# Kernel tuning notes

Hardware: AMD Instinct MI355X
Metric: run time of the kernel (lower is better)

## Reference

```python
import jax, jax.numpy as jnp
import numpy as np

HEADS = 5 - 1  # 4 attention heads (GPSConv heads=4)


def _bn(x, g, b, eps=1e-5):
    # BatchNorm1d, training-mode math (biased variance), matches torch normalization
    mu = x.mean(0)
    var = x.var(0)
    return g * (x - mu) * jax.lax.rsqrt(var + eps) + b


def _forward(x, t, freqs, t_fc1_W, t_fc1_b, t_fc2_W, t_fc2_b, node_W, node_b,
             tproj_W, tproj_b, tcat_W, tcat_b, pen_g, pen_b, pel_W, pel_b,
             cat_W, cat_b, conv_Wg, gru_Wih, gru_bih, gru_Whh, gru_bhh,
             attn_Wqkv, attn_bqkv, attn_Wo, attn_bo, bn_g, bn_b,
             mlp_W1, mlp_b1, mlp_W2, mlp_b2, out_W, out_b):
    B, C, Hh, Ww = x.shape
    HD = node_W.shape[1]          # hidden_dim = 64
    DH = HD // HEADS              # per-head dim = 16
    WL = pen_g.shape[0]           # walk_length = 20

    xf = x.reshape(B, -1)                              # [B, D]
    h = xf @ node_W + node_b                           # node_proj

    # TimeEmbedding: t @ freqs -> sin/cos -> MLP, then time_proj
    tp = t.reshape(B, 1) * freqs.reshape(1, -1)        # [B, nf]
    two_pi = jnp.asarray(2.0 * np.pi, x.dtype)
    te = jnp.concatenate([jnp.sin(two_pi * tp), jnp.cos(two_pi * tp)], axis=-1)
    te = jax.nn.silu(te @ t_fc1_W + t_fc1_b) @ t_fc2_W + t_fc2_b
    h_time = te @ tproj_W + tproj_b
    h = jnp.concatenate([h, h_time], axis=-1) @ tcat_W + tcat_b  # time_cat_proj

    # Fully-connected graph incl. self-loops: A = 1 everywhere, deg = B.
    # Random-walk PE: P = A/deg has all entries 1/B; P is idempotent (P@P = P),
    # hence diag(P^k) = diag(P) = 1/B for every k in 1..walk_length.
    A = jnp.ones((B, B), x.dtype)
    P = A / A.sum(1, keepdims=True)
    pe = jnp.broadcast_to(jnp.diagonal(P)[:, None], (B, WL))
    pe = _bn(pe, pen_g, pen_b)                         # pe_norm (batch stats)
    h = jnp.concatenate([h, pe @ pel_W + pel_b], axis=-1) @ cat_W + cat_b

    inv_sqrt = jnp.asarray(1.0 / np.sqrt(DH), x.dtype)
    for l in range(conv_Wg.shape[0]):                  # 5 GPSConv layers
        # --- GatedGraphConv (num_layers=1): message, add-aggregate, GRU ---
        m = A @ (h @ conv_Wg[l])                       # sum of messages from all src nodes
        gi = m @ gru_Wih[l] + gru_bih[l]               # [B, 3H]
        gh = h @ gru_Whh[l] + gru_bhh[l]
        ir, iz, inn = jnp.split(gi, 3, axis=-1)
        hr, hz, hn = jnp.split(gh, 3, axis=-1)
        r = jax.nn.sigmoid(ir + hr)
        z = jax.nn.sigmoid(iz + hz)
        n = jnp.tanh(inn + r * hn)
        hc = (1.0 - z) * n + z * h                     # GRUCell output
        h1 = _bn(hc + h, bn_g[l, 0], bn_b[l, 0])       # residual + norm1

        # --- global multihead self-attention over the single dense batch ---
        qkv = h @ attn_Wqkv[l] + attn_bqkv[l]
        q, k, v = jnp.split(qkv, 3, axis=-1)
        q = q.reshape(B, HEADS, DH).transpose(1, 0, 2)  # [h, B, d]
        k = k.reshape(B, HEADS, DH).transpose(1, 0, 2)
        v = v.reshape(B, HEADS, DH).transpose(1, 0, 2)
        att = jax.nn.softmax(jnp.einsum('hqd,hkd->hqk', q, k) * inv_sqrt, axis=-1)
        o = jnp.einsum('hqk,hkd->hqd', att, v).transpose(1, 0, 2).reshape(B, HD)
        o = o @ attn_Wo[l] + attn_bo[l]
        h2 = _bn(o + h, bn_g[l, 1], bn_b[l, 1])        # residual + norm2

        s = h1 + h2
        s = s + (jax.nn.relu(s @ mlp_W1[l] + mlp_b1[l]) @ mlp_W2[l] + mlp_b2[l])
        h = _bn(s, bn_g[l, 2], bn_b[l, 2])             # norm3

    return (h @ out_W + out_b).reshape(B, C, Hh, Ww)


def setup_inputs() -> dict:
    key = jax.random.key(0)
    B, C, H, W = 2048, 4, 32, 32
    D = C * H * W                 # 4096
    HD, PE, WL, L = 64, 16, 20, 5
    NF, TH, TC = 8, 64, 64
    ks = iter(jax.random.split(key, 40))

    def rn(shape, s=0.05):
        return jax.random.normal(next(ks), shape, jnp.float32) * s

    return {
        'x': jax.random.normal(next(ks), (B, C, H, W), jnp.float32),
        't': jax.random.uniform(next(ks), (B,), jnp.float32),
        'freqs': rn((NF,), 1.0),
        't_fc1_W': rn((2 * NF, TH)), 't_fc1_b': rn((TH,)),
        't_fc2_W': rn((TH, TC)), 't_fc2_b': rn((TC,)),
        'node_W': rn((D, HD), 0.02), 'node_b': rn((HD,)),
        'tproj_W': rn((TC, HD)), 'tproj_b': rn((HD,)),
        'tcat_W': rn((2 * HD, HD)), 'tcat_b': rn((HD,)),
        'pen_g': jnp.ones((WL,), jnp.float32), 'pen_b': jnp.zeros((WL,), jnp.float32),
        'pel_W': rn((WL, PE)), 'pel_b': rn((PE,)),
        'cat_W': rn((HD + PE, HD)), 'cat_b': rn((HD,)),
        'conv_Wg': rn((L, HD, HD)),
        'gru_Wih': rn((L, HD, 3 * HD)), 'gru_bih': rn((L, 3 * HD)),
        'gru_Whh': rn((L, HD, 3 * HD)), 'gru_bhh': rn((L, 3 * HD)),
        'attn_Wqkv': rn((L, HD, 3 * HD)), 'attn_bqkv': rn((L, 3 * HD)),
        'attn_Wo': rn((L, HD, HD)), 'attn_bo': rn((L, HD)),
        'bn_g': jnp.ones((L, 3, HD), jnp.float32), 'bn_b': jnp.zeros((L, 3, HD), jnp.float32),
        'mlp_W1': rn((L, HD, 2 * HD)), 'mlp_b1': rn((L, 2 * HD)),
        'mlp_W2': rn((L, 2 * HD, HD)), 'mlp_b2': rn((L, HD)),
        'out_W': rn((HD, D)), 'out_b': rn((D,)),
    }


def reference(x, t, freqs, t_fc1_W, t_fc1_b, t_fc2_W, t_fc2_b, node_W, node_b,
              tproj_W, tproj_b, tcat_W, tcat_b, pen_g, pen_b, pel_W, pel_b,
              cat_W, cat_b, conv_Wg, gru_Wih, gru_bih, gru_Whh, gru_bhh,
              attn_Wqkv, attn_bqkv, attn_Wo, attn_bo, bn_g, bn_b,
              mlp_W1, mlp_b1, mlp_W2, mlp_b2, out_W, out_b):
    return _forward(x, t, freqs, t_fc1_W, t_fc1_b, t_fc2_W, t_fc2_b, node_W, node_b,
                    tproj_W, tproj_b, tcat_W, tcat_b, pen_g, pen_b, pel_W, pel_b,
                    cat_W, cat_b, conv_Wg, gru_Wih, gru_bih, gru_Whh, gru_bhh,
                    attn_Wqkv, attn_bqkv, attn_Wo, attn_bo, bn_g, bn_b,
                    mlp_W1, mlp_b1, mlp_W2, mlp_b2, out_W, out_b)
```

## Files before the change

### kernel.cpp

```cpp
#include <hip/hip_runtime.h>

#define NB 2048
#define HDM 64
#define NLAY 5

typedef __bf16 bf16x8 __attribute__((ext_vector_type(8)));
typedef float v4f __attribute__((ext_vector_type(4)));

__device__ __forceinline__ float sigmoidf_(float x){ return 1.f/(1.f+__expf(-x)); }
__device__ __forceinline__ float tanhfast_(float x){
  x = fminf(fmaxf(x, -15.f), 15.f);
  float e = __expf(2.f*x);
  return (e-1.f)/(e+1.f);
}
__device__ __forceinline__ unsigned short f2b_rne(float f){
  unsigned u = __float_as_uint(f);
  unsigned r = u + 0x7FFFu + ((u>>16)&1u);
  return (unsigned short)(r>>16);
}
__device__ __forceinline__ unsigned pk2(float a, float b){
  unsigned ua = (__float_as_uint(a) + 0x8000u) >> 16;
  unsigned ub = (__float_as_uint(b) + 0x8000u) & 0xFFFF0000u;
  return ua | ub;
}

__global__ __launch_bounds__(256) void k_pre(
    const float* __restrict__ x, const float* __restrict__ tt,
    const float* __restrict__ freqs,
    const float* __restrict__ fc1W, const float* __restrict__ fc1b,
    const float* __restrict__ fc2W, const float* __restrict__ fc2b,
    const float* __restrict__ tprojW, const float* __restrict__ tprojb,
    const float* __restrict__ nodeW,
    float* __restrict__ h0p, float* __restrict__ htime,
    float* __restrict__ zero_region)
{
  __shared__ float xs[16*260];
  __shared__ float tb0[128];
  __shared__ float tb1[128];
  const int t = threadIdx.x, blk = blockIdx.x;
  const int r = t>>6, c = t&63;

  if (blk == 0){
    for (int i = t; i < 320 + 1920; i += 256) zero_region[i] = 0.f;
  }

  {
    const int row = blk*2 + (r&1);
    const float tv = tt[row];
    if (r < 2){
      float te[16];
      #pragma unroll
      for (int j=0;j<8;++j){
        float sv, cv;
        __sincosf(6.28318530717958647692f*tv*freqs[j], &sv, &cv);
        te[j]=sv; te[j+8]=cv;
      }
      float a = fc1b[c];
      #pragma unroll
      for (int j=0;j<16;++j) a += te[j]*fc1W[j*64+c];
      tb0[r*64+c] = a*sigmoidf_(a);
    }
    __syncthreads();
    if (r < 2){
      float b2 = fc2b[c];
      #pragma unroll 8
      for (int k=0;k<64;++k) b2 += tb0[r*64+k]*fc2W[k*64+c];
      tb1[r*64+c] = b2;
    }
    __syncthreads();
    if (r < 2){
      float hti = tprojb[c];
      #pragma unroll 8
      for (int k=0;k<64;++k) hti += tb1[r*64+k]*tprojW[k*64+c];
      htime[row*64+c] = hti;
    }
  }

  const int rg = blk>>3, kq = blk&7;
  const int rows0 = rg*16, k0 = kq*512;
  const int col4 = (t&15)*4;
  const int rq4  = ((t>>4)&3)*4;
  const int ksub = (t>>6)*64;

  float4 a0={0,0,0,0}, a1={0,0,0,0}, a2={0,0,0,0}, a3={0,0,0,0};

  for (int ch=0; ch<2; ++ch){
    __syncthreads();
    #pragma unroll
    for (int i=0;i<4;++i){
      int fi = t + 256*i;
      int xr = fi>>6, kk = (fi&63)<<2;
      *(float4*)&xs[xr*260+kk] = *(const float4*)&x[(size_t)(rows0+xr)*4096 + k0 + ch*256 + kk];
    }
    __syncthreads();
    const float* wp = &nodeW[(size_t)(k0 + ch*256 + ksub)*64 + col4];
    const float* xp = &xs[rq4*260 + ksub];
    #pragma unroll 8
    for (int kk=0; kk<64; ++kk){
      float4 w  = *(const float4*)&wp[kk*64];
      float x0 = xp[kk];
      float x1 = xp[260+kk];
      float x2 = xp[520+kk];
      float x3 = xp[780+kk];
      a0.x += x0*w.x; a0.y += x0*w.y; a0.z += x0*w.z; a0.w += x0*w.w;
      a1.x += x1*w.x; a1.y += x1*w.y; a1.z += x1*w.z; a1.w += x1*w.w;
      a2.x += x2*w.x; a2.y += x2*w.y; a2.z += x2*w.z; a2.w += x2*w.w;
      a3.x += x3*w.x; a3.y += x3*w.y; a3.z += x3*w.z; a3.w += x3*w.w;
    }
  }
  __syncthreads();
  {
    const int kqi = t>>6;
    *(float4*)&xs[(kqi*16 + rq4 + 0)*64 + col4] = a0;
    *(float4*)&xs[(kqi*16 + rq4 + 1)*64 + col4] = a1;
    *(float4*)&xs[(kqi*16 + rq4 + 2)*64 + col4] = a2;
    *(float4*)&xs[(kqi*16 + rq4 + 3)*64 + col4] = a3;
  }
  __syncthreads();
  {
    const int row = t>>4, c4 = (t&15)*4;
    float4 s = {0,0,0,0};
    #pragma unroll
    for (int q=0;q<4;++q){
      float4 v = *(const float4*)&xs[(q*16+row)*64 + c4];
      s.x+=v.x; s.y+=v.y; s.z+=v.z; s.w+=v.w;
    }
    *(float4*)&h0p[(size_t)kq*(NB*HDM) + (rows0+row)*64 + c4] = s;
  }
}

__global__ __launch_bounds__(256) void k_assemble(
    const float* __restrict__ h0p, const float* __restrict__ htime,
    const float* __restrict__ nodeb,
    const float* __restrict__ tcatW, const float* __restrict__ tcatb,
    const float* __restrict__ penb, const float* __restrict__ pelW,
    const float* __restrict__ pelb,
    const float* __restrict__ catW, const float* __restrict__ catb,
    float* __restrict__ hbuf)
{
  __shared__ float sa[256];
  __shared__ float sb[256];
  __shared__ float cvec[64];
  const int t = threadIdx.x, blk = blockIdx.x;
  const int r = t>>6, c = t&63;
  const int row = blk*4 + r;

  if (r==0){
    float pl[16];
    #pragma unroll
    for (int j=0;j<16;++j){
      float a = pelb[j];
      for (int w=0;w<20;++w) a += penb[w]*pelW[w*16+j];
      pl[j]=a;
    }
    float a = catb[c];
    #pragma unroll
    for (int j=0;j<16;++j) a += pl[j]*catW[(64+j)*64+c];
    cvec[c]=a;
  }
  float h0 = nodeb[c];
  #pragma unroll
  for (int q=0;q<8;++q) h0 += h0p[(size_t)q*(NB*HDM) + row*64 + c];
  sa[t] = h0;
  sb[t] = htime[row*64+c];
  __syncthreads();
  float a = tcatb[c];
  #pragma unroll 4
  for (int k=0;k<64;++k){
    a += sa[r*64+k]*tcatW[k*64+c];
    a += sb[r*64+k]*tcatW[(64+k)*64+c];
  }
  __syncthreads();
  sa[t] = a;
  __syncthreads();
  float hv = cvec[c];
  #pragma unroll 8
  for (int k=0;k<64;++k) hv += sa[r*64+k]*catW[k*64+c];
  hbuf[row*64+c] = hv;
}

__global__ __launch_bounds__(256) void k_A(
    const float* __restrict__ smlp,
    const float* __restrict__ bnaccPrev,
    const float* __restrict__ gPrev, const float* __restrict__ bPrev,
    float* __restrict__ hbuf, float* __restrict__ hsumL,
    const float* __restrict__ Whh, const float* __restrict__ bhh,
    const float* __restrict__ Wq,  const float* __restrict__ bq,
    float* __restrict__ gh,
    unsigned short* __restrict__ Qb, unsigned short* __restrict__ Kb,
    unsigned short* __restrict__ Vt, int first)
{
  __shared__ float sa[8*64];
  const int t = threadIdx.x, blk = blockIdx.x;
  const int row0 = blk*8;

  #pragma unroll
  for (int i=0;i<2;++i){
    int idx = t + 256*i;
    int rl = idx>>6, c = idx&63;
    int row = row0 + rl;
    float hv;
    if (first){
      hv = hbuf[row*64+c];
    } else {
      float mu = bnaccPrev[256+c]*(1.f/NB);
      float va = bnaccPrev[320+c]*(1.f/NB) - mu*mu;
      hv = gPrev[c]*(smlp[row*64+c]-mu)*rsqrtf(va+1e-5f)+bPrev[c];
      hbuf[row*64+c] = hv;
    }
    sa[idx] = hv;
  }
  __syncthreads();
  if (t<64){
    float s = 0.f;
    #pragma unroll
    for (int rl=0;rl<8;++rl) s += sa[rl*64+t];
    atomicAdd(&hsumL[t], s);
  }
  if (t < 192){
    const int cc = t;
    float ag[8], aq[8];
    float bh = bhh[cc], bq_ = bq[cc];
    #pragma unroll
    for (int rl=0;rl<8;++rl){ ag[rl]=bh; aq[rl]=bq_; }
    #pragma unroll 4
    for (int k=0;k<64;++k){
      float wh = Whh[k*192+cc];
      float wq = Wq [k*192+cc];
      #pragma unroll
      for (int rl=0;rl<8;++rl){
        float hk = sa[rl*64+k];
        ag[rl] += hk*wh;
        aq[rl] += hk*wq;
      }
    }
    #pragma unroll
    for (int rl=0;rl<8;++rl){
      int rw = row0 + rl;
      gh[(size_t)rw*192+cc] = ag[rl];
      float aqv = aq[rl];
      if (cc < 64){
        int hd = cc>>4, dh = cc&15;
        size_t base = ((size_t)(hd<<11) + rw)*32;
        Qb[base+dh] = f2b_rne(aqv*0.25f);
        Qb[base+16+dh] = 0;
      } else if (cc < 128){
        int c2 = cc-64, hd = c2>>4, dh = c2&15;
        size_t base = ((size_t)(hd<<11) + rw)*32;
        Kb[base+dh] = f2b_rne(aqv);
        Kb[base+16+dh] = 0;
      } else {
        int c2 = cc-128, hd = c2>>4, dh = c2&15;
        Vt[((size_t)(hd*16+dh))*2048 + rw] = f2b_rne(aqv);
      }
    }
  }
}

__global__ __launch_bounds__(256) void k_attn(
    const unsigned short* __restrict__ Qb, const unsigned short* __restrict__ Kb,
    const unsigned short* __restrict__ Vt,
    float* __restrict__ o_out)
{
  __shared__ unsigned short Pl[4*640];
  __shared__ float Os[4*272];
  __shared__ float ms[64], ls[64];
  const int t = threadIdx.x;
  const int w = t>>6, lane = t&63;
  const int q15 = lane & 15, quad = lane >> 4;
  const int b = blockIdx.x;
  const int qt = b & 127, head = b>>7;
  const int qrow = qt*16 + q15;
  const int key00 = w*512;
  unsigned short* Plw = &Pl[w*640];

  const bf16x8 qf = *(const bf16x8*)&Qb[(((size_t)(head<<11))+qrow)*32 + quad*8];
  const unsigned short* Kb_h = Kb + ((size_t)(head<<11))*32;
  const unsigned short* Vrow = Vt + ((size_t)(head*16+q15))*2048;

  v4f O = {0.f,0.f,0.f,0.f};
  float m = -1e30f, lsum = 0.f;

  bf16x8 kf0 = *(const bf16x8*)&Kb_h[(size_t)(key00 + q15)*32 + quad*8];
  bf16x8 kf1 = *(const bf16x8*)&Kb_h[(size_t)(key00 + 16 + q15)*32 + quad*8];
  bf16x8 vf  = *(const bf16x8*)&Vrow[key00 + quad*8];

  for (int c=0; c<16; ++c){
    bf16x8 nk0, nk1, nv;
    if (c < 15){
      int nk = key00 + (c+1)*32;
      nk0 = *(const bf16x8*)&Kb_h[(size_t)(nk + q15)*32 + quad*8];
      nk1 = *(const bf16x8*)&Kb_h[(size_t)(nk + 16 + q15)*32 + quad*8];
      nv  = *(const bf16x8*)&Vrow[nk + quad*8];
    }
    v4f z = {0.f,0.f,0.f,0.f};
    v4f s0 = __builtin_amdgcn_mfma_f32_16x16x32_bf16(kf0, qf, z, 0,0,0);
    v4f s1 = __builtin_amdgcn_mfma_f32_16x16x32_bf16(kf1, qf, z, 0,0,0);
    float cmax = fmaxf(fmaxf(fmaxf(s0[0],s0[1]),fmaxf(s0[2],s0[3])),
                       fmaxf(fmaxf(s1[0],s1[1]),fmaxf(s1[2],s1[3])));
    cmax = fmaxf(cmax, __shfl_xor(cmax,16,64));
    cmax = fmaxf(cmax, __shfl_xor(cmax,32,64));
    float mnew = fmaxf(m, cmax);
    float alpha = __expf(m - mnew);
    float p0=__expf(s0[0]-mnew), p1=__expf(s0[1]-mnew), p2=__expf(s0[2]-mnew), p3=__expf(s0[3]-mnew);
    float p4=__expf(s1[0]-mnew), p5=__expf(s1[1]-mnew), p6=__expf(s1[2]-mnew), p7=__expf(s1[3]-mnew);
    lsum = alpha*lsum + ((p0+p1)+(p2+p3)+((p4+p5)+(p6+p7)));
    m = mnew;
    O[0]*=alpha; O[1]*=alpha; O[2]*=alpha; O[3]*=alpha;
    *(uint2*)&Plw[q15*40 + quad*4]      = make_uint2(pk2(p0,p1), pk2(p2,p3));
    *(uint2*)&Plw[q15*40 + 16 + quad*4] = make_uint2(pk2(p4,p5), pk2(p6,p7));
    asm volatile("s_waitcnt lgkmcnt(0)" ::: "memory");
    bf16x8 pf = *(const bf16x8*)&Plw[q15*40 + quad*8];
    O = __builtin_amdgcn_mfma_f32_16x16x32_bf16(vf, pf, O, 0,0,0);
    kf0 = nk0; kf1 = nk1; vf = nv;
  }
  lsum += __shfl_xor(lsum,16,64);
  lsum += __shfl_xor(lsum,32,64);
  #pragma unroll
  for (int j=0;j<4;++j) Os[w*272 + q15*17 + quad*4 + j] = O[j];
  if (quad==0){ ms[w*16+q15]=m; ls[w*16+q15]=lsum; }
  __syncthreads();
  {
    const int dh = t&15, q = t>>4;
    float m0=ms[q], m1=ms[16+q], m2=ms[32+q], m3=ms[48+q];
    float mm = fmaxf(fmaxf(m0,m1),fmaxf(m2,m3));
    float a0=__expf(m0-mm), a1=__expf(m1-mm), a2=__expf(m2-mm), a3=__expf(m3-mm);
    float ll = a0*ls[q]+a1*ls[16+q]+a2*ls[32+q]+a3*ls[48+q];
    float oo = a0*Os[q*17+dh] + a1*Os[272+q*17+dh] + a2*Os[544+q*17+dh] + a3*Os[816+q*17+dh];
    o_out[(size_t)(qt*16+q)*64 + head*16 + dh] = oo / ll;
  }
}

__global__ __launch_bounds__(256) void k_B2(
    const float* __restrict__ hbuf, const float* __restrict__ gh,
    const float* __restrict__ hsumL, const float* __restrict__ o_out,
    const float* __restrict__ Wg,   const float* __restrict__ Wih,
    const float* __restrict__ bih,  const float* __restrict__ Wo,
    const float* __restrict__ bo,
    float* __restrict__ s1, float* __restrict__ s2, float* __restrict__ bnaccL)
{
  __shared__ float sa[8*64];
  __shared__ float os[8*64];
  __shared__ float smv_[64];
  __shared__ float sgi[192];
  __shared__ float Sb1[8*64];
  __shared__ float Sb2[8*64];
  const int t = threadIdx.x, blk = blockIdx.x;
  const int row0 = blk*8;

  if (t<64){
    float a=0.f;
    #pragma unroll 8
    for (int k=0;k<64;++k) a += hsumL[k]*Wg[k*64+t];
    smv_[t]=a;
  }
  #pragma unroll
  for (int i=0;i<2;++i){
    int idx = t + 256*i;
    int rl = idx>>6, c = idx&63;
    sa[idx] = hbuf[(size_t)(row0+rl)*64+c];
    os[idx] = o_out[(size_t)(row0+rl)*64+c];
  }
  __syncthreads();
  if (t<192){
    float a = bih[t];
    #pragma unroll 8
    for (int k=0;k<64;++k) a += smv_[k]*Wih[k*192+t];
    sgi[t]=a;
  }
  __syncthreads();

  const int c = t&63, rg = t>>6;
  float o2a = bo[c], o2b = bo[c];
  #pragma unroll 4
  for (int k=0;k<64;++k){
    float w = Wo[k*64+c];
    o2a += os[(rg*2  )*64+k]*w;
    o2b += os[(rg*2+1)*64+k]*w;
  }
  #pragma unroll
  for (int i=0;i<2;++i){
    int rl = rg*2 + i;
    int row = row0 + rl;
    float o2 = i ? o2b : o2a;
    float hv = sa[rl*64+c];
    float s2v = o2 + hv;
    float ir = sgi[c]      + gh[(size_t)row*192+c];
    float iz = sgi[64+c]   + gh[(size_t)row*192+64+c];
    float inn = sgi[128+c];
    float hn  = gh[(size_t)row*192+128+c];
    float rr_ = sigmoidf_(ir);
    float zz  = sigmoidf_(iz);
    float nn  = tanhfast_(inn + rr_*hn);
    float s1v = (1.f-zz)*nn + zz*hv + hv;
    s1[(size_t)row*64+c] = s1v;
    s2[(size_t)row*64+c] = s2v;
    Sb1[rl*64+c] = s1v;
    Sb2[rl*64+c] = s2v;
  }
  __syncthreads();
  if (t<64){
    float a=0.f,aq=0.f,b=0.f,bq2=0.f;
    #pragma unroll
    for (int rl=0;rl<8;++rl){
      float v1 = Sb1[rl*64+t], v2 = Sb2[rl*64+t];
      a+=v1; aq+=v1*v1; b+=v2; bq2+=v2*v2;
    }
    atomicAdd(&bnaccL[t],a);     atomicAdd(&bnaccL[64+t],aq);
    atomicAdd(&bnaccL[128+t],b); atomicAdd(&bnaccL[192+t],bq2);
  }
}

__global__ __launch_bounds__(256) void k_C(
    const float* __restrict__ s1, const float* __restrict__ s2,
    const float* __restrict__ bngL, const float* __restrict__ bnbL,
    const float* __restrict__ W1, const float* __restrict__ b1,
    const float* __restrict__ W2, const float* __restrict__ b2,
    float* __restrict__ smlp, float* __restrict__ bnaccL)
{
  __shared__ float sa[8*64];
  __shared__ float sh[8*128];
  __shared__ float S2[8*64];
  const int t = threadIdx.x, blk = blockIdx.x;
  const int row0 = blk*8;

  #pragma unroll
  for (int i=0;i<2;++i){
    int idx = t + 256*i;
    int rl = idx>>6, c = idx&63;
    int row = row0 + rl;
    float mu1 = bnaccL[c]*(1.f/NB);
    float va1 = bnaccL[64+c]*(1.f/NB) - mu1*mu1;
    float mu2 = bnaccL[128+c]*(1.f/NB);
    float va2 = bnaccL[192+c]*(1.f/NB) - mu2*mu2;
    float h1 = bngL[c]*(s1[(size_t)row*64+c]-mu1)*rsqrtf(va1+1e-5f)+bnbL[c];
    float h2 = bngL[64+c]*(s2[(size_t)row*64+c]-mu2)*rsqrtf(va2+1e-5f)+bnbL[64+c];
    sa[idx] = h1+h2;
  }
  __syncthreads();
  {
    const int hj = t&127, rgq = t>>7;
    float a0v=b1[hj], a1v=b1[hj], a2v=b1[hj], a3v=b1[hj];
    #pragma unroll 4
    for (int k=0;k<64;++k){
      float w = W1[k*128+hj];
      a0v += sa[(rgq*4  )*64+k]*w;
      a1v += sa[(rgq*4+1)*64+k]*w;
      a2v += sa[(rgq*4+2)*64+k]*w;
      a3v += sa[(rgq*4+3)*64+k]*w;
    }
    sh[(rgq*4  )*128+hj] = fmaxf(a0v,0.f);
    sh[(rgq*4+1)*128+hj] = fmaxf(a1v,0.f);
    sh[(rgq*4+2)*128+hj] = fmaxf(a2v,0.f);
    sh[(rgq*4+3)*128+hj] = fmaxf(a3v,0.f);
  }
  __syncthreads();
  {
    const int c = t&63, rg = t>>6;
    float moa = b2[c], mob = b2[c];
    #pragma unroll 4
    for (int k=0;k<128;++k){
      float w = W2[k*64+c];
      moa += sh[(rg*2  )*128+k]*w;
      mob += sh[(rg*2+1)*128+k]*w;
    }
    #pragma unroll
    for (int i=0;i<2;++i){
      int rl = rg*2+i;
      float smv2 = sa[rl*64+c] + (i ? mob : moa);
      smlp[(size_t)(row0+rl)*64+c] = smv2;
      S2[rl*64+c] = smv2;
    }
  }
  __syncthreads();
  if (t<64){
    float a=0.f,aq=0.f;
    #pragma unroll
    for (int rl=0;rl<8;++rl){ float v=S2[rl*64+t]; a+=v; aq+=v*v; }
    atomicAdd(&bnaccL[256+t],a); atomicAdd(&bnaccL[320+t],aq);
  }
}

__global__ __launch_bounds__(256) void k_out(
  const float* __restrict__ smlp, const float* __restrict__ bnacc4,
  const float* __restrict__ g4, const float* __restrict__ b4,
  const float* __restrict__ outW, const float* __restrict__ outb,
  float* __restrict__ out)
{
  __shared__ float hsT[64*20];
  const int t = threadIdx.x, blk = blockIdx.x;
  const int rg = blk>>2, cg = blk&3;
  const int rows0 = rg*16;
  #pragma unroll
  for (int i=0;i<4;++i){
    int idx = t + 256*i;
    int k = idx&63, rr = idx>>6;
    float mu = bnacc4[256+k]*(1.f/NB);
    float va = bnacc4[320+k]*(1.f/NB)-mu*mu;
    hsT[k*20+rr] = g4[k]*(smlp[(size_t)(rows0+rr)*64+k]-mu)*rsqrtf(va+1e-5f)+b4[k];
  }
  __syncthreads();
  const int cc = cg*1024 + t*4;
  float4 acc[16];
  {
    float4 bv = *(const float4*)&outb[cc];
    #pragma unroll
    for (int rr=0;rr<16;++rr) acc[rr]=bv;
  }
  #pragma unroll 4
  for (int k=0;k<64;++k){
    float4 w = *(const float4*)&outW[(size_t)k*4096+cc];
    const float4* hp = (const float4*)&hsT[k*20];
    float4 h0=hp[0], h1=hp[1], h2=hp[2], h3=hp[3];
    acc[0].x+=h0.x*w.x;  acc[0].y+=h0.x*w.y;  acc[0].z+=h0.x*w.z;  acc[0].w+=h0.x*w.w;
    acc[1].x+=h0.y*w.x;  acc[1].y+=h0.y*w.y;  acc[1].z+=h0.y*w.z;  acc[1].w+=h0.y*w.w;
    acc[2].x+=h0.z*w.x;  acc[2].y+=h0.z*w.y;  acc[2].z+=h0.z*w.z;  acc[2].w+=h0.z*w.w;
    acc[3].x+=h0.w*w.x;  acc[3].y+=h0.w*w.y;  acc[3].z+=h0.w*w.z;  acc[3].w+=h0.w*w.w;
    acc[4].x+=h1.x*w.x;  acc[4].y+=h1.x*w.y;  acc[4].z+=h1.x*w.z;  acc[4].w+=h1.x*w.w;
    acc[5].x+=h1.y*w.x;  acc[5].y+=h1.y*w.y;  acc[5].z+=h1.y*w.z;  acc[5].w+=h1.y*w.w;
    acc[6].x+=h1.z*w.x;  acc[6].y+=h1.z*w.y;  acc[6].z+=h1.z*w.z;  acc[6].w+=h1.z*w.w;
    acc[7].x+=h1.w*w.x;  acc[7].y+=h1.w*w.y;  acc[7].z+=h1.w*w.z;  acc[7].w+=h1.w*w.w;
    acc[8].x+=h2.x*w.x;  acc[8].y+=h2.x*w.y;  acc[8].z+=h2.x*w.z;  acc[8].w+=h2.x*w.w;
    acc[9].x+=h2.y*w.x;  acc[9].y+=h2.y*w.y;  acc[9].z+=h2.y*w.z;  acc[9].w+=h2.y*w.w;
    acc[10].x+=h2.z*w.x; acc[10].y+=h2.z*w.y; acc[10].z+=h2.z*w.z; acc[10].w+=h2.z*w.w;
    acc[11].x+=h2.w*w.x; acc[11].y+=h2.w*w.y; acc[11].z+=h2.w*w.z; acc[11].w+=h2.w*w.w;
    acc[12].x+=h3.x*w.x; acc[12].y+=h3.x*w.y; acc[12].z+=h3.x*w.z; acc[12].w+=h3.x*w.w;
    acc[13].x+=h3.y*w.x; acc[13].y+=h3.y*w.y; acc[13].z+=h3.y*w.z; acc[13].w+=h3.y*w.w;
    acc[14].x+=h3.z*w.x; acc[14].y+=h3.z*w.y; acc[14].z+=h3.z*w.z; acc[14].w+=h3.z*w.w;
    acc[15].x+=h3.w*w.x; acc[15].y+=h3.w*w.y; acc[15].z+=h3.w*w.z; acc[15].w+=h3.w*w.w;
  }
  #pragma unroll
  for (int rr=0;rr<16;++rr)
    *(float4*)&out[(size_t)(rows0+rr)*4096+cc] = acc[rr];
}

extern "C" void kernel_launch(void* const* d_in, const int* in_sizes, int n_in,
                              void* d_out, int out_size, void* d_ws, size_t ws_size,
                              hipStream_t stream)
{
  (void)in_sizes; (void)n_in; (void)out_size; (void)ws_size;
  const float* x      = (const float*)d_in[0];
  const float* tt     = (const float*)d_in[1];
  const float* freqs  = (const float*)d_in[2];
  const float* fc1W   = (const float*)d_in[3];
  const float* fc1b   = (const float*)d_in[4];
  const float* fc2W   = (const float*)d_in[5];
  const float* fc2b   = (const float*)d_in[6];
  const float* nodeW  = (const float*)d_in[7];
  const float* nodeb  = (const float*)d_in[8];
  const float* tprojW = (const float*)d_in[9];
  const float* tprojb = (const float*)d_in[10];
  const float* tcatW  = (const float*)d_in[11];
  const float* tcatb  = (const float*)d_in[12];
  const float* penb   = (const float*)d_in[14];
  const float* pelW   = (const float*)d_in[15];
  const float* pelb   = (const float*)d_in[16];
  const float* catW   = (const float*)d_in[17];
  const float* catb   = (const float*)d_in[18];
  const float* convWg = (const float*)d_in[19];
  const float* gruWih = (const float*)d_in[20];
  const float* grubih = (const float*)d_in[21];
  const float* gruWhh = (const float*)d_in[22];
  const float* grubhh = (const float*)d_in[23];
  const float* Wqkv   = (const float*)d_in[24];
  const float* bqkv   = (const float*)d_in[25];
  const float* Wo     = (const float*)d_in[26];
  const float* bo     = (const float*)d_in[27];
  const float* bng    = (const float*)d_in[28];
  const float* bnb    = (const float*)d_in[29];
  const float* W1     = (const float*)d_in[30];
  const float* b1     = (const float*)d_in[31];
  const float* W2     = (const float*)d_in[32];
  const float* b2     = (const float*)d_in[33];
  const float* outW   = (const float*)d_in[34];
  const float* outb   = (const float*)d_in[35];

  float* ws = (float*)d_ws;
  float* htime = ws;
  float* hbuf  = htime + 131072;
  float* gh    = hbuf + 131072;
  float* s1    = gh + 393216;
  float* s2    = s1 + 131072;
  float* smlp  = s2 + 131072;
  float* o_out = smlp + 131072;
  float* hsum  = o_out + 131072;
  float* bnacc = hsum + 320;
  unsigned short* Qb = (unsigned short*)(bnacc + 1920);
  unsigned short* Kb = Qb + 262144;
  unsigned short* Vt = Kb + 262144;
  float* h0p  = (float*)(Vt + 65536);

  dim3 Blk(256);

  k_pre<<<dim3(1024), Blk, 0, stream>>>(x, tt, freqs, fc1W, fc1b, fc2W, fc2b,
                                        tprojW, tprojb, nodeW, h0p, htime, hsum);

  k_assemble<<<dim3(512), Blk, 0, stream>>>(h0p, htime, nodeb, tcatW, tcatb,
                                            penb, pelW, pelb, catW, catb, hbuf);

  for (int l=0; l<NLAY; ++l){
    const float* bnaccPrev = (l==0) ? bnacc : bnacc + (l-1)*384;
    const float* gPrev = (l==0) ? bng : bng + (l-1)*192 + 128;
    const float* bPrev = (l==0) ? bnb : bnb + (l-1)*192 + 128;
    k_A<<<dim3(256), Blk, 0, stream>>>(smlp, bnaccPrev, gPrev, bPrev,
                                       hbuf, hsum + l*64,
                                       gruWhh + l*12288, grubhh + l*192,
                                       Wqkv + l*12288, bqkv + l*192,
                                       gh, Qb, Kb, Vt, (l==0) ? 1 : 0);
    k_attn<<<dim3(512), Blk, 0, stream>>>(Qb, Kb, Vt, o_out);
    k_B2<<<dim3(256), Blk, 0, stream>>>(hbuf, gh, hsum + l*64, o_out,
                                        convWg + l*4096, gruWih + l*12288, grubih + l*192,
                                        Wo + l*4096, bo + l*64,
                                        s1, s2, bnacc + l*384);
    k_C<<<dim3(256), Blk, 0, stream>>>(s1, s2, bng + l*192, bnb + l*192,
                                       W1 + l*8192, b1 + l*128, W2 + l*8192, b2 + l*64,
                                       smlp, bnacc + l*384);
  }

  k_out<<<dim3(512), Blk, 0, stream>>>(smlp, bnacc + 4*384, bng + 896, bnb + 896,
                                       outW, outb, (float*)d_out);
}
```

Measured before the change: 523.5 us.

## Fuse all stages into one persistent megakernel with grid-wide barriers

```diff
diff --git a/kernel.cpp b/kernel.cpp
--- a/kernel.cpp
+++ b/kernel.cpp
@@ -24,514 +24,438 @@
   return ua | ub;
 }
 
-__global__ __launch_bounds__(256) void k_pre(
-    const float* __restrict__ x, const float* __restrict__ tt,
-    const float* __restrict__ freqs,
-    const float* __restrict__ fc1W, const float* __restrict__ fc1b,
-    const float* __restrict__ fc2W, const float* __restrict__ fc2b,
-    const float* __restrict__ tprojW, const float* __restrict__ tprojb,
-    const float* __restrict__ nodeW,
-    float* __restrict__ h0p, float* __restrict__ htime,
-    float* __restrict__ zero_region)
+struct MP {
+  const float *x, *tt, *freqs, *fc1W, *fc1b, *fc2W, *fc2b, *tprojW, *tprojb;
+  const float *nodeW, *nodeb, *tcatW, *tcatb, *penb, *pelW, *pelb, *catW, *catb;
+  const float *convWg, *gruWih, *grubih, *gruWhh, *grubhh;
+  const float *Wqkv, *bqkv, *Wo, *bo, *bng, *bnb, *W1, *b1, *W2, *b2, *outW, *outb;
+  float *out;
+  unsigned *cnt;
+  float *hsum;
+  float *bnacc;
+  unsigned short *Kb, *Vt;
+  float *h0p;
+  float *smlpG;
+};
+
+__device__ __forceinline__ void gbar(unsigned* cnt, unsigned& ph){
+  __syncthreads();
+  if (threadIdx.x == 0){
+    ph += 1;
+    unsigned tgt = ph * 256u;
+    __hip_atomic_fetch_add(cnt, 1u, __ATOMIC_ACQ_REL, __HIP_MEMORY_SCOPE_AGENT);
+    while (__hip_atomic_load(cnt, __ATOMIC_ACQUIRE, __HIP_MEMORY_SCOPE_AGENT) < tgt)
+      __builtin_amdgcn_s_sleep(2);
+  }
+  __syncthreads();
+}
+
+__global__ __launch_bounds__(512) void k_mega(MP p)
 {
-  __shared__ float xs[16*260];
-  __shared__ float tb0[128];
-  __shared__ float tb1[128];
+  __shared__ float LDSf[11264];
+  float* hL    = LDSf;
+  float* ghL   = LDSf + 512;
+  float* qL    = LDSf + 2048;
+  float* smlpL = LDSf + 2560;
+  float* TR    = LDSf + 3072;
+
   const int t = threadIdx.x, blk = blockIdx.x;
-  const int r = t>>6, c = t&63;
-
-  if (blk == 0){
-    for (int i = t; i < 320 + 1920; i += 256) zero_region[i] = 0.f;
+  const int row0 = blk*8;
+  unsigned bph = 0;
+
+  {
+    const int rt = blk>>1, kq = blk&1;
+    const int rows0 = rt*16, k0 = kq*2048;
+    const int col4 = (t&15)*4, rq4 = ((t>>4)&3)*4, ks = t>>6;
+    float4 a0={0,0,0,0}, a1={0,0,0,0}, a2={0,0,0,0}, a3={0,0,0,0};
+    for (int ch=0; ch<8; ++ch){
+      __syncthreads();
+      #pragma unroll
+      for (int i=0;i<2;++i){
+        int fi = t + 512*i;
+        int xr = fi>>6, kk = (fi&63)<<2;
+        *(float4*)&TR[xr*260+kk] = *(const float4*)&p.x[(size_t)(rows0+xr)*4096 + k0 + ch*256 + kk];
+      }
+      __syncthreads();
+      const float* wp = &p.nodeW[(size_t)(k0 + ch*256 + ks*32)*64 + col4];
+      const float* xp = &TR[rq4*260 + ks*32];
+      #pragma unroll 8
+      for (int kk=0; kk<32; ++kk){
+        float4 w = *(const float4*)&wp[kk*64];
+        float x0 = xp[kk], x1 = xp[260+kk], x2 = xp[520+kk], x3 = xp[780+kk];
+        a0.x += x0*w.x; a0.y += x0*w.y; a0.z += x0*w.z; a0.w += x0*w.w;
+        a1.x += x1*w.x; a1.y += x1*w.y; a1.z += x1*w.z; a1.w += x1*w.w;
+        a2.x += x2*w.x; a2.y += x2*w.y; a2.z += x2*w.z; a2.w += x2*w.w;
+        a3.x += x3*w.x; a3.y += x3*w.y; a3.z += x3*w.z; a3.w += x3*w.w;
+      }
+    }
+    __syncthreads();
+    *(float4*)&TR[ks*1024 + (rq4+0)*64 + col4] = a0;
+    *(float4*)&TR[ks*1024 + (rq4+1)*64 + col4] = a1;
+    *(float4*)&TR[ks*1024 + (rq4+2)*64 + col4] = a2;
+    *(float4*)&TR[ks*1024 + (rq4+3)*64 + col4] = a3;
+    __syncthreads();
+    if (t < 256){
+      int row = t>>4, c4 = (t&15)*4;
+      float4 s = {0,0,0,0};
+      #pragma unroll
+      for (int q=0;q<8;++q){
+        float4 v = *(const float4*)&TR[q*1024 + row*64 + c4];
+        s.x+=v.x; s.y+=v.y; s.z+=v.z; s.w+=v.w;
+      }
+      *(float4*)&p.h0p[(size_t)kq*(NB*64) + (size_t)(rows0+row)*64 + c4] = s;
+    }
   }
-
-  {
-    const int row = blk*2 + (r&1);
-    const float tv = tt[row];
-    if (r < 2){
+  gbar(p.cnt, bph);
+
+  for (int l=0; l<NLAY; ++l){
+    if (l == 0){
+      float* tb0 = TR;        float* tb1 = TR+512;
+      float* htL = TR+1024;   float* h0L = TR+1536;
+      float* hcat= TR+2048;   float* cvec= TR+2560;
+      const int r = t>>6, c = t&63;
+      const int row = row0 + r;
+      float tv = p.tt[row];
       float te[16];
       #pragma unroll
       for (int j=0;j<8;++j){
         float sv, cv;
-        __sincosf(6.28318530717958647692f*tv*freqs[j], &sv, &cv);
+        __sincosf(6.28318530717958647692f*tv*p.freqs[j], &sv, &cv);
         te[j]=sv; te[j+8]=cv;
       }
-      float a = fc1b[c];
+      float a = p.fc1b[c];
       #pragma unroll
-      for (int j=0;j<16;++j) a += te[j]*fc1W[j*64+c];
+      for (int j=0;j<16;++j) a += te[j]*p.fc1W[j*64+c];
       tb0[r*64+c] = a*sigmoidf_(a);
+      h0L[r*64+c] = p.nodeb[c] + p.h0p[(size_t)row*64+c] + p.h0p[(size_t)NB*64 + (size_t)row*64+c];
+      if (t < 64){
+        float pl[16];
+        #pragma unroll
+        for (int j=0;j<16;++j){
+          float pa = p.pelb[j];
+          for (int wv=0;wv<20;++wv) pa += p.penb[wv]*p.pelW[wv*16+j];
+          pl[j]=pa;
+        }
+        float cv = p.catb[t];
+        #pragma unroll
+        for (int j=0;j<16;++j) cv += pl[j]*p.catW[(64+j)*64+t];
+        cvec[t]=cv;
+      }
+      __syncthreads();
+      float b2v = p.fc2b[c];
+      #pragma unroll 8
+      for (int k=0;k<64;++k) b2v += tb0[r*64+k]*p.fc2W[k*64+c];
+      tb1[r*64+c] = b2v;
+      __syncthreads();
+      float ht = p.tprojb[c];
+      #pragma unroll 8
+      for (int k=0;k<64;++k) ht += tb1[r*64+k]*p.tprojW[k*64+c];
+      htL[r*64+c] = ht;
+      __syncthreads();
+      float ac = p.tcatb[c];
+      #pragma unroll 4
+      for (int k=0;k<64;++k){
+        ac += h0L[r*64+k]*p.tcatW[k*64+c];
+        ac += htL[r*64+k]*p.tcatW[(64+k)*64+c];
+      }
+      hcat[r*64+c] = ac;
+      __syncthreads();
+      float hv = cvec[c];
+      #pragma unroll 8
+      for (int k=0;k<64;++k) hv += hcat[r*64+k]*p.catW[k*64+c];
+      hL[r*64+c] = hv;
+      __syncthreads();
+      if (t < 64){
+        float s = 0.f;
+        #pragma unroll
+        for (int rl=0;rl<8;++rl) s += hL[rl*64+t];
+        atomicAdd(&p.hsum[t], s);
+      }
+    } else {
+      const float* stp = p.bnacc + (l-1)*384;
+      const float* gP = p.bng + (l-1)*192 + 128;
+      const float* bP = p.bnb + (l-1)*192 + 128;
+      const int c = t&63, rg = t>>6;
+      float mu = stp[256+c]*(1.f/NB);
+      float va = stp[320+c]*(1.f/NB) - mu*mu;
+      hL[rg*64+c] = gP[c]*(smlpL[rg*64+c]-mu)*rsqrtf(va+1e-5f)+bP[c];
+      __syncthreads();
+    }
+    {
+      int grp = -1, cc = 0;
+      if (t < 192){ grp = 0; cc = t; }
+      else if (t >= 256 && t < 448){ grp = 1; cc = t-256; }
+      if (grp >= 0){
+        const float* Whh = p.gruWhh + l*12288;
+        const float* Wq  = p.Wqkv  + l*12288;
+        float ag[4], aq[4];
+        float bh = p.grubhh[l*192+cc], bqv = p.bqkv[l*192+cc];
+        #pragma unroll
+        for (int rl=0;rl<4;++rl){ ag[rl]=bh; aq[rl]=bqv; }
+        const int rb = grp*4;
+        #pragma unroll 4
+        for (int k=0;k<64;++k){
+          float wh = Whh[k*192+cc];
+          float wq = Wq [k*192+cc];
+          #pragma unroll
+          for (int rl=0;rl<4;++rl){
+            float hk = hL[(rb+rl)*64+k];
+            ag[rl] += hk*wh;
+            aq[rl] += hk*wq;
+          }
+        }
+        #pragma unroll
+        for (int rl=0;rl<4;++rl){
+          int r4 = rb+rl, rw = row0 + r4;
+          ghL[r4*192+cc] = ag[rl];
+          float av = aq[rl];
+          if (cc < 64){
+            qL[r4*64+cc] = av;
+          } else if (cc < 128){
+            int c2 = cc-64, hd = c2>>4, dh = c2&15;
+            size_t base = ((size_t)(hd<<11) + rw)*32;
+            p.Kb[base+dh] = f2b_rne(av);
+            p.Kb[base+16+dh] = 0;
+          } else {
+            int c2 = cc-128, hd = c2>>4, dh = c2&15;
+            p.Vt[((size_t)(hd*16+dh))*2048 + rw] = f2b_rne(av);
+          }
+        }
+      }
+    }
+    gbar(p.cnt, bph);
+
+    {
+      float* smv = TR;     float* gi = TR+64;
+      if (t < 64){
+        const float* Wg = p.convWg + l*4096;
+        float a = 0.f;
+        if (l == 0){
+          #pragma unroll 8
+          for (int k=0;k<64;++k) a += p.hsum[k]*Wg[k*64+t];
+        } else {
+          const float* bP = p.bnb + (l-1)*192 + 128;
+          #pragma unroll 8
+          for (int k=0;k<64;++k) a += (2048.f*bP[k])*Wg[k*64+t];
+        }
+        smv[t]=a;
+      }
+      __syncthreads();
+      if (t < 192){
+        const float* Wih = p.gruWih + l*12288;
+        float a = p.grubih[l*192+t];
+        #pragma unroll 8
+        for (int k=0;k<64;++k) a += smv[k]*Wih[k*192+t];
+        gi[t]=a;
+      }
+      {
+        const int w = t>>6, lane = t&63;
+        const int q15 = lane&15, quad = lane>>4;
+        const int head = w>>1, e = w&1;
+        const int key00 = e*1024;
+        unsigned short* Plw = (unsigned short*)(TR+256) + w*640;
+        bf16x8 qf;
+        {
+          unsigned short* qp = (unsigned short*)&qf;
+          #pragma unroll
+          for (int j=0;j<8;++j){
+            int dh = quad*8+j;
+            float v = (q15 < 8 && dh < 16) ? qL[q15*64 + head*16 + dh]*0.25f : 0.f;
+            qp[j] = f2b_rne(v);
+          }
+        }
+        const unsigned short* Kb_h = p.Kb + ((size_t)(head<<11))*32;
+        const unsigned short* Vrow = p.Vt + ((size_t)(head*16+q15))*2048;
+        v4f O = {0.f,0.f,0.f,0.f};
+        float m = -1e30f, lsum = 0.f;
+        bf16x8 kf0 = *(const bf16x8*)&Kb_h[(size_t)(key00 + q15)*32 + quad*8];
+        bf16x8 kf1 = *(const bf16x8*)&Kb_h[(size_t)(key00 + 16 + q15)*32 + quad*8];
+        bf16x8 vf  = *(const bf16x8*)&Vrow[key00 + quad*8];
+        for (int c=0; c<32; ++c){
+          bf16x8 nk0, nk1, nv;
+          if (c < 31){
+            int nk = key00 + (c+1)*32;
+            nk0 = *(const bf16x8*)&Kb_h[(size_t)(nk + q15)*32 + quad*8];
+            nk1 = *(const bf16x8*)&Kb_h[(size_t)(nk + 16 + q15)*32 + quad*8];
+            nv  = *(const bf16x8*)&Vrow[nk + quad*8];
+          }
+          v4f z = {0.f,0.f,0.f,0.f};
+          v4f s0 = __builtin_amdgcn_mfma_f32_16x16x32_bf16(kf0, qf, z, 0,0,0);
+          v4f s1 = __builtin_amdgcn_mfma_f32_16x16x32_bf16(kf1, qf, z, 0,0,0);
+          float cmax = fmaxf(fmaxf(fmaxf(s0[0],s0[1]),fmaxf(s0[2],s0[3])),
+                             fmaxf(fmaxf(s1[0],s1[1]),fmaxf(s1[2],s1[3])));
+          cmax = fmaxf(cmax, __shfl_xor(cmax,16,64));
+          cmax = fmaxf(cmax, __shfl_xor(cmax,32,64));
+          float mnew = fmaxf(m, cmax);
+          float alpha = __expf(m - mnew);
+          float p0=__expf(s0[0]-mnew), p1=__expf(s0[1]-mnew), p2=__expf(s0[2]-mnew), p3=__expf(s0[3]-mnew);
+          float p4=__expf(s1[0]-mnew), p5=__expf(s1[1]-mnew), p6=__expf(s1[2]-mnew), p7=__expf(s1[3]-mnew);
+          lsum = alpha*lsum + ((p0+p1)+(p2+p3)+((p4+p5)+(p6+p7)));
+          m = mnew;
+          O[0]*=alpha; O[1]*=alpha; O[2]*=alpha; O[3]*=alpha;
+          *(uint2*)&Plw[q15*40 + quad*4]      = make_uint2(pk2(p0,p1), pk2(p2,p3));
+          *(uint2*)&Plw[q15*40 + 16 + quad*4] = make_uint2(pk2(p4,p5), pk2(p6,p7));
+          asm volatile("s_waitcnt lgkmcnt(0)" ::: "memory");
+          bf16x8 pf = *(const bf16x8*)&Plw[q15*40 + quad*8];
+          O = __builtin_amdgcn_mfma_f32_16x16x32_bf16(vf, pf, O, 0,0,0);
+          kf0 = nk0; kf1 = nk1; vf = nv;
+        }
+        lsum += __shfl_xor(lsum,16,64);
+        lsum += __shfl_xor(lsum,32,64);
+        float* Os = TR+2816; float* ms = TR+4992; float* ls = TR+5120;
+        #pragma unroll
+        for (int j=0;j<4;++j) Os[w*272 + q15*17 + quad*4 + j] = O[j];
+        if (quad==0){ ms[w*16+q15]=m; ls[w*16+q15]=lsum; }
+      }
+      __syncthreads();
+      {
+        float* Os = TR+2816; float* ms = TR+4992; float* ls = TR+5120; float* oL = TR+5248;
+        const int q = t>>6, c = t&63;
+        const int head = c>>4, dh = c&15;
+        const int w0 = head*2, w1 = w0+1;
+        float m0 = ms[w0*16+q], m1 = ms[w1*16+q];
+        float mm = fmaxf(m0,m1);
+        float a0 = __expf(m0-mm), a1 = __expf(m1-mm);
+        float ll = a0*ls[w0*16+q] + a1*ls[w1*16+q];
+        float oo = a0*Os[w0*272+q*17+dh] + a1*Os[w1*272+q*17+dh];
+        oL[q*64+c] = oo / ll;
+      }
+      __syncthreads();
+      {
+        float* oL = TR+5248; float* Sb1 = TR+5760; float* Sb2 = TR+6272;
+        const int c = t&63, rg = t>>6;
+        const float* Wo = p.Wo + l*4096;
+        float o2 = p.bo[l*64+c];
+        #pragma unroll 8
+        for (int k=0;k<64;++k) o2 += oL[rg*64+k]*Wo[k*64+c];
+        float hv = hL[rg*64+c];
+        float s2v = o2 + hv;
+        float ir  = gi[c]      + ghL[rg*192+c];
+        float iz  = gi[64+c]   + ghL[rg*192+64+c];
+        float inn = gi[128+c];
+        float hn  = ghL[rg*192+128+c];
+        float rr_ = sigmoidf_(ir);
+        float zz  = sigmoidf_(iz);
+        float nn  = tanhfast_(inn + rr_*hn);
+        float s1v = (1.f-zz)*nn + zz*hv + hv;
+        Sb1[rg*64+c] = s1v;
+        Sb2[rg*64+c] = s2v;
+      }
+      __syncthreads();
+      if (t < 64){
+        float* Sb1 = TR+5760; float* Sb2 = TR+6272;
+        float* st = p.bnacc + l*384;
+        float a=0.f,aq=0.f,b=0.f,bq2=0.f;
+        #pragma unroll
+        for (int rl=0;rl<8;++rl){
+          float v1 = Sb1[rl*64+t], v2 = Sb2[rl*64+t];
+          a+=v1; aq+=v1*v1; b+=v2; bq2+=v2*v2;
+        }
+        atomicAdd(&st[t],a);     atomicAdd(&st[64+t],aq);
+        atomicAdd(&st[128+t],b); atomicAdd(&st[192+t],bq2);
+      }
+    }
+    gbar(p.cnt, bph);
+
+    {
+      float* sa = TR; float* sh = TR+512;
+      float* Sb1 = TR+5760; float* Sb2 = TR+6272;
+      const float* st = p.bnacc + l*384;
+      const float* bngL = p.bng + l*192;
+      const float* bnbL = p.bnb + l*192;
+      const int c = t&63, rg = t>>6;
+      float mu1 = st[c]*(1.f/NB);
+      float va1 = st[64+c]*(1.f/NB) - mu1*mu1;
+      float mu2 = st[128+c]*(1.f/NB);
+      float va2 = st[192+c]*(1.f/NB) - mu2*mu2;
+      float h1 = bngL[c]*(Sb1[rg*64+c]-mu1)*rsqrtf(va1+1e-5f)+bnbL[c];
+      float h2 = bngL[64+c]*(Sb2[rg*64+c]-mu2)*rsqrtf(va2+1e-5f)+bnbL[64+c];
+      sa[rg*64+c] = h1+h2;
+      __syncthreads();
+      {
+        const float* W1 = p.W1 + l*8192;
+        const int hj = t&127, rq = t>>7;
+        float aA = p.b1[l*128+hj], aB = aA;
+        #pragma unroll 4
+        for (int k=0;k<64;++k){
+          float w = W1[k*128+hj];
+          aA += sa[(rq*2  )*64+k]*w;
+          aB += sa[(rq*2+1)*64+k]*w;
+        }
+        sh[(rq*2  )*128+hj] = fmaxf(aA,0.f);
+        sh[(rq*2+1)*128+hj] = fmaxf(aB,0.f);
+      }
+      __syncthreads();
+      {
+        const float* W2 = p.W2 + l*8192;
+        float mo = p.b2[l*64+c];
+        #pragma unroll 8
+        for (int k=0;k<128;++k) mo += sh[rg*128+k]*W2[k*64+c];
+        float sm = sa[rg*64+c] + mo;
+        smlpL[rg*64+c] = sm;
+        if (l == NLAY-1) p.smlpG[(size_t)(row0+rg)*64+c] = sm;
+      }
+      __syncthreads();
+      if (t < 64){
+        float* st2 = p.bnacc + l*384;
+        float a=0.f,aq=0.f;
+        #pragma unroll
+        for (int rl=0;rl<8;++rl){ float v = smlpL[rl*64+t]; a+=v; aq+=v*v; }
+        atomicAdd(&st2[256+t],a); atomicAdd(&st2[320+t],aq);
+      }
+    }
+    gbar(p.cnt, bph);
+  }
+
+  {
+    const int rt = blk>>1, chf = blk&1;
+    const int rows0 = rt*16;
+    float* hsT = TR;
+    const float* st = p.bnacc + 4*384;
+    const float* g4 = p.bng + 4*192 + 128;
+    const float* b4 = p.bnb + 896;
+    #pragma unroll
+    for (int i=0;i<2;++i){
+      int idx = t + 512*i;
+      int k = idx&63, rr = idx>>6;
+      float mu = st[256+k]*(1.f/NB);
+      float va = st[320+k]*(1.f/NB) - mu*mu;
+      hsT[k*20+rr] = g4[k]*(p.smlpG[(size_t)(rows0+rr)*64+k]-mu)*rsqrtf(va+1e-5f)+b4[k];
     }
     __syncthreads();
-    if (r < 2){
-      float b2 = fc2b[c];
-      #pragma unroll 8
-      for (int k=0;k<64;++k) b2 += tb0[r*64+k]*fc2W[k*64+c];
-      tb1[r*64+c] = b2;
-    }
-    __syncthreads();
-    if (r < 2){
-      float hti = tprojb[c];
-      #pragma unroll 8
-      for (int k=0;k<64;++k) hti += tb1[r*64+k]*tprojW[k*64+c];
-      htime[row*64+c] = hti;
-    }
-  }
-
-  const int rg = blk>>3, kq = blk&7;
-  const int rows0 = rg*16, k0 = kq*512;
-  const int col4 = (t&15)*4;
-  const int rq4  = ((t>>4)&3)*4;
-  const int ksub = (t>>6)*64;
-
-  float4 a0={0,0,0,0}, a1={0,0,0,0}, a2={0,0,0,0}, a3={0,0,0,0};
-
-  for (int ch=0; ch<2; ++ch){
-    __syncthreads();
-    #pragma unroll
-    for (int i=0;i<4;++i){
-      int fi = t + 256*i;
-      int xr = fi>>6, kk = (fi&63)<<2;
-      *(float4*)&xs[xr*260+kk] = *(const float4*)&x[(size_t)(rows0+xr)*4096 + k0 + ch*256 + kk];
-    }
-    __syncthreads();
-    const float* wp = &nodeW[(size_t)(k0 + ch*256 + ksub)*64 + col4];
-    const float* xp = &xs[rq4*260 + ksub];
-    #pragma unroll 8
-    for (int kk=0; kk<64; ++kk){
-      float4 w  = *(const float4*)&wp[kk*64];
-      float x0 = xp[kk];
-      float x1 = xp[260+kk];
-      float x2 = xp[520+kk];
-      float x3 = xp[780+kk];
-      a0.x += x0*w.x; a0.y += x0*w.y; a0.z += x0*w.z; a0.w += x0*w.w;
-      a1.x += x1*w.x; a1.y += x1*w.y; a1.z += x1*w.z; a1.w += x1*w.w;
-      a2.x += x2*w.x; a2.y += x2*w.y; a2.z += x2*w.z; a2.w += x2*w.w;
-      a3.x += x3*w.x; a3.y += x3*w.y; a3.z += x3*w.z; a3.w += x3*w.w;
-    }
-  }
-  __syncthreads();
-  {
-    const int kqi = t>>6;
-    *(float4*)&xs[(kqi*16 + rq4 + 0)*64 + col4] = a0;
-    *(float4*)&xs[(kqi*16 + rq4 + 1)*64 + col4] = a1;
-    *(float4*)&xs[(kqi*16 + rq4 + 2)*64 + col4] = a2;
-    *(float4*)&xs[(kqi*16 + rq4 + 3)*64 + col4] = a3;
-  }
-  __syncthreads();
-  {
-    const int row = t>>4, c4 = (t&15)*4;
-    float4 s = {0,0,0,0};
-    #pragma unroll
-    for (int q=0;q<4;++q){
-      float4 v = *(const float4*)&xs[(q*16+row)*64 + c4];
-      s.x+=v.x; s.y+=v.y; s.z+=v.z; s.w+=v.w;
-    }
-    *(float4*)&h0p[(size_t)kq*(NB*HDM) + (rows0+row)*64 + c4] = s;
-  }
-}
-
-__global__ __launch_bounds__(256) void k_assemble(
-    const float* __restrict__ h0p, const float* __restrict__ htime,
-    const float* __restrict__ nodeb,
-    const float* __restrict__ tcatW, const float* __restrict__ tcatb,
-    const float* __restrict__ penb, const float* __restrict__ pelW,
-    const float* __restrict__ pelb,
-    const float* __restrict__ catW, const float* __restrict__ catb,
-    float* __restrict__ hbuf)
-{
-  __shared__ float sa[256];
-  __shared__ float sb[256];
-  __shared__ float cvec[64];
-  const int t = threadIdx.x, blk = blockIdx.x;
-  const int r = t>>6, c = t&63;
-  const int row = blk*4 + r;
-
-  if (r==0){
-    float pl[16];
-    #pragma unroll
-    for (int j=0;j<16;++j){
-      float a = pelb[j];
-      for (int w=0;w<20;++w) a += penb[w]*pelW[w*16+j];
-      pl[j]=a;
-    }
-    float a = catb[c];
-    #pragma unroll
-    for (int j=0;j<16;++j) a += pl[j]*catW[(64+j)*64+c];
-    cvec[c]=a;
-  }
-  float h0 = nodeb[c];
-  #pragma unroll
-  for (int q=0;q<8;++q) h0 += h0p[(size_t)q*(NB*HDM) + row*64 + c];
-  sa[t] = h0;
-  sb[t] = htime[row*64+c];
-  __syncthreads();
-  float a = tcatb[c];
-  #pragma unroll 4
-  for (int k=0;k<64;++k){
-    a += sa[r*64+k]*tcatW[k*64+c];
-    a += sb[r*64+k]*tcatW[(64+k)*64+c];
-  }
-  __syncthreads();
-  sa[t] = a;
-  __syncthreads();
-  float hv = cvec[c];
-  #pragma unroll 8
-  for (int k=0;k<64;++k) hv += sa[r*64+k]*catW[k*64+c];
-  hbuf[row*64+c] = hv;
-}
-
-__global__ __launch_bounds__(256) void k_A(
-    const float* __restrict__ smlp,
-    const float* __restrict__ bnaccPrev,
-    const float* __restrict__ gPrev, const float* __restrict__ bPrev,
-    float* __restrict__ hbuf, float* __restrict__ hsumL,
-    const float* __restrict__ Whh, const float* __restrict__ bhh,
-    const float* __restrict__ Wq,  const float* __restrict__ bq,
-    float* __restrict__ gh,
-    unsigned short* __restrict__ Qb, unsigned short* __restrict__ Kb,
-    unsigned short* __restrict__ Vt, int first)
-{
-  __shared__ float sa[8*64];
-  const int t = threadIdx.x, blk = blockIdx.x;
-  const int row0 = blk*8;
-
-  #pragma unroll
-  for (int i=0;i<2;++i){
-    int idx = t + 256*i;
-    int rl = idx>>6, c = idx&63;
-    int row = row0 + rl;
-    float hv;
-    if (first){
-      hv = hbuf[row*64+c];
-    } else {
-      float mu = bnaccPrev[256+c]*(1.f/NB);
-      float va = bnaccPrev[320+c]*(1.f/NB) - mu*mu;
-      hv = gPrev[c]*(smlp[row*64+c]-mu)*rsqrtf(va+1e-5f)+bPrev[c];
-      hbuf[row*64+c] = hv;
-    }
-    sa[idx] = hv;
-  }
-  __syncthreads();
-  if (t<64){
-    float s = 0.f;
-    #pragma unroll
-    for (int rl=0;rl<8;++rl) s += sa[rl*64+t];
-    atomicAdd(&hsumL[t], s);
-  }
-  if (t < 192){
-    const int cc = t;
-    float ag[8], aq[8];
-    float bh = bhh[cc], bq_ = bq[cc];
-    #pragma unroll
-    for (int rl=0;rl<8;++rl){ ag[rl]=bh; aq[rl]=bq_; }
+    const int cc = chf*2048 + t*4;
+    float4 acc[16];
+    {
+      float4 bv = *(const float4*)&p.outb[cc];
+      #pragma unroll
+      for (int rr=0;rr<16;++rr) acc[rr]=bv;
+    }
     #pragma unroll 4
     for (int k=0;k<64;++k){
-      float wh = Whh[k*192+cc];
-      float wq = Wq [k*192+cc];
-      #pragma unroll
-      for (int rl=0;rl<8;++rl){
-        float hk = sa[rl*64+k];
-        ag[rl] += hk*wh;
-        aq[rl] += hk*wq;
-      }
+      float4 w = *(const float4*)&p.outW[(size_t)k*4096+cc];
+      const float4* hp = (const float4*)&hsT[k*20];
+      float4 h0=hp[0], h1=hp[1], h2=hp[2], h3=hp[3];
+      acc[0].x+=h0.x*w.x;  acc[0].y+=h0.x*w.y;  acc[0].z+=h0.x*w.z;  acc[0].w+=h0.x*w.w;
+      acc[1].x+=h0.y*w.x;  acc[1].y+=h0.y*w.y;  acc[1].z+=h0.y*w.z;  acc[1].w+=h0.y*w.w;
+      acc[2].x+=h0.z*w.x;  acc[2].y+=h0.z*w.y;  acc[2].z+=h0.z*w.z;  acc[2].w+=h0.z*w.w;
+      acc[3].x+=h0.w*w.x;  acc[3].y+=h0.w*w.y;  acc[3].z+=h0.w*w.z;  acc[3].w+=h0.w*w.w;
+      acc[4].x+=h1.x*w.x;  acc[4].y+=h1.x*w.y;  acc[4].z+=h1.x*w.z;  acc[4].w+=h1.x*w.w;
+      acc[5].x+=h1.y*w.x;  acc[5].y+=h1.y*w.y;  acc[5].z+=h1.y*w.z;  acc[5].w+=h1.y*w.w;
+      acc[6].x+=h1.z*w.x;  acc[6].y+=h1.z*w.y;  acc[6].z+=h1.z*w.z;  acc[6].w+=h1.z*w.w;
+      acc[7].x+=h1.w*w.x;  acc[7].y+=h1.w*w.y;  acc[7].z+=h1.w*w.z;  acc[7].w+=h1.w*w.w;
+      acc[8].x+=h2.x*w.x;  acc[8].y+=h2.x*w.y;  acc[8].z+=h2.x*w.z;  acc[8].w+=h2.x*w.w;
+      acc[9].x+=h2.y*w.x;  acc[9].y+=h2.y*w.y;  acc[9].z+=h2.y*w.z;  acc[9].w+=h2.y*w.w;
+      acc[10].x+=h2.z*w.x; acc[10].y+=h2.z*w.y; acc[10].z+=h2.z*w.z; acc[10].w+=h2.z*w.w;
+      acc[11].x+=h2.w*w.x; acc[11].y+=h2.w*w.y; acc[11].z+=h2.w*w.z; acc[11].w+=h2.w*w.w;
+      acc[12].x+=h3.x*w.x; acc[12].y+=h3.x*w.y; acc[12].z+=h3.x*w.z; acc[12].w+=h3.x*w.w;
+      acc[13].x+=h3.y*w.x; acc[13].y+=h3.y*w.y; acc[13].z+=h3.y*w.z; acc[13].w+=h3.y*w.w;
+      acc[14].x+=h3.z*w.x; acc[14].y+=h3.z*w.y; acc[14].z+=h3.z*w.z; acc[14].w+=h3.z*w.w;
+      acc[15].x+=h3.w*w.x; acc[15].y+=h3.w*w.y; acc[15].z+=h3.w*w.z; acc[15].w+=h3.w*w.w;
     }
     #pragma unroll
-    for (int rl=0;rl<8;++rl){
-      int rw = row0 + rl;
-      gh[(size_t)rw*192+cc] = ag[rl];
-      float aqv = aq[rl];
-      if (cc < 64){
-        int hd = cc>>4, dh = cc&15;
-        size_t base = ((size_t)(hd<<11) + rw)*32;
-        Qb[base+dh] = f2b_rne(aqv*0.25f);
-        Qb[base+16+dh] = 0;
-      } else if (cc < 128){
-        int c2 = cc-64, hd = c2>>4, dh = c2&15;
-        size_t base = ((size_t)(hd<<11) + rw)*32;
-        Kb[base+dh] = f2b_rne(aqv);
-        Kb[base+16+dh] = 0;
-      } else {
-        int c2 = cc-128, hd = c2>>4, dh = c2&15;
-        Vt[((size_t)(hd*16+dh))*2048 + rw] = f2b_rne(aqv);
-      }
-    }
+    for (int rr=0;rr<16;++rr)
+      *(float4*)&p.out[(size_t)(rows0+rr)*4096+cc] = acc[rr];
   }
-}
-
-__global__ __launch_bounds__(256) void k_attn(
-    const unsigned short* __restrict__ Qb, const unsigned short* __restrict__ Kb,
-    const unsigned short* __restrict__ Vt,
-    float* __restrict__ o_out)
-{
-  __shared__ unsigned short Pl[4*640];
-  __shared__ float Os[4*272];
-  __shared__ float ms[64], ls[64];
-  const int t = threadIdx.x;
-  const int w = t>>6, lane = t&63;
-  const int q15 = lane & 15, quad = lane >> 4;
-  const int b = blockIdx.x;
-  const int qt = b & 127, head = b>>7;
-  const int qrow = qt*16 + q15;
-  const int key00 = w*512;
-  unsigned short* Plw = &Pl[w*640];
-
-  const bf16x8 qf = *(const bf16x8*)&Qb[(((size_t)(head<<11))+qrow)*32 + quad*8];
-  const unsigned short* Kb_h = Kb + ((size_t)(head<<11))*32;
-  const unsigned short* Vrow = Vt + ((size_t)(head*16+q15))*2048;
-
-  v4f O = {0.f,0.f,0.f,0.f};
-  float m = -1e30f, lsum = 0.f;
-
-  bf16x8 kf0 = *(const bf16x8*)&Kb_h[(size_t)(key00 + q15)*32 + quad*8];
-  bf16x8 kf1 = *(const bf16x8*)&Kb_h[(size_t)(key00 + 16 + q15)*32 + quad*8];
-  bf16x8 vf  = *(const bf16x8*)&Vrow[key00 + quad*8];
-
-  for (int c=0; c<16; ++c){
-    bf16x8 nk0, nk1, nv;
-    if (c < 15){
-      int nk = key00 + (c+1)*32;
-      nk0 = *(const bf16x8*)&Kb_h[(size_t)(nk + q15)*32 + quad*8];
-      nk1 = *(const bf16x8*)&Kb_h[(size_t)(nk + 16 + q15)*32 + quad*8];
-      nv  = *(const bf16x8*)&Vrow[nk + quad*8];
-    }
-    v4f z = {0.f,0.f,0.f,0.f};
-    v4f s0 = __builtin_amdgcn_mfma_f32_16x16x32_bf16(kf0, qf, z, 0,0,0);
-    v4f s1 = __builtin_amdgcn_mfma_f32_16x16x32_bf16(kf1, qf, z, 0,0,0);
-    float cmax = fmaxf(fmaxf(fmaxf(s0[0],s0[1]),fmaxf(s0[2],s0[3])),
-                       fmaxf(fmaxf(s1[0],s1[1]),fmaxf(s1[2],s1[3])));
-    cmax = fmaxf(cmax, __shfl_xor(cmax,16,64));
-    cmax = fmaxf(cmax, __shfl_xor(cmax,32,64));
-    float mnew = fmaxf(m, cmax);
-    float alpha = __expf(m - mnew);
-    float p0=__expf(s0[0]-mnew), p1=__expf(s0[1]-mnew), p2=__expf(s0[2]-mnew), p3=__expf(s0[3]-mnew);
-    float p4=__expf(s1[0]-mnew), p5=__expf(s1[1]-mnew), p6=__expf(s1[2]-mnew), p7=__expf(s1[3]-mnew);
-    lsum = alpha*lsum + ((p0+p1)+(p2+p3)+((p4+p5)+(p6+p7)));
-    m = mnew;
-    O[0]*=alpha; O[1]*=alpha; O[2]*=alpha; O[3]*=alpha;
-    *(uint2*)&Plw[q15*40 + quad*4]      = make_uint2(pk2(p0,p1), pk2(p2,p3));
-    *(uint2*)&Plw[q15*40 + 16 + quad*4] = make_uint2(pk2(p4,p5), pk2(p6,p7));
-    asm volatile("s_waitcnt lgkmcnt(0)" ::: "memory");
-    bf16x8 pf = *(const bf16x8*)&Plw[q15*40 + quad*8];
-    O = __builtin_amdgcn_mfma_f32_16x16x32_bf16(vf, pf, O, 0,0,0);
-    kf0 = nk0; kf1 = nk1; vf = nv;
-  }
-  lsum += __shfl_xor(lsum,16,64);
-  lsum += __shfl_xor(lsum,32,64);
-  #pragma unroll
-  for (int j=0;j<4;++j) Os[w*272 + q15*17 + quad*4 + j] = O[j];
-  if (quad==0){ ms[w*16+q15]=m; ls[w*16+q15]=lsum; }
-  __syncthreads();
-  {
-    const int dh = t&15, q = t>>4;
-    float m0=ms[q], m1=ms[16+q], m2=ms[32+q], m3=ms[48+q];
-    float mm = fmaxf(fmaxf(m0,m1),fmaxf(m2,m3));
-    float a0=__expf(m0-mm), a1=__expf(m1-mm), a2=__expf(m2-mm), a3=__expf(m3-mm);
-    float ll = a0*ls[q]+a1*ls[16+q]+a2*ls[32+q]+a3*ls[48+q];
-    float oo = a0*Os[q*17+dh] + a1*Os[272+q*17+dh] + a2*Os[544+q*17+dh] + a3*Os[816+q*17+dh];
-    o_out[(size_t)(qt*16+q)*64 + head*16 + dh] = oo / ll;
-  }
-}
-
-__global__ __launch_bounds__(256) void k_B2(
-    const float* __restrict__ hbuf, const float* __restrict__ gh,
-    const float* __restrict__ hsumL, const float* __restrict__ o_out,
-    const float* __restrict__ Wg,   const float* __restrict__ Wih,
-    const float* __restrict__ bih,  const float* __restrict__ Wo,
-    const float* __restrict__ bo,
-    float* __restrict__ s1, float* __restrict__ s2, float* __restrict__ bnaccL)
-{
-  __shared__ float sa[8*64];
-  __shared__ float os[8*64];
-  __shared__ float smv_[64];
-  __shared__ float sgi[192];
-  __shared__ float Sb1[8*64];
-  __shared__ float Sb2[8*64];
-  const int t = threadIdx.x, blk = blockIdx.x;
-  const int row0 = blk*8;
-
-  if (t<64){
-    float a=0.f;
-    #pragma unroll 8
-    for (int k=0;k<64;++k) a += hsumL[k]*Wg[k*64+t];
-    smv_[t]=a;
-  }
-  #pragma unroll
-  for (int i=0;i<2;++i){
-    int idx = t + 256*i;
-    int rl = idx>>6, c = idx&63;
-    sa[idx] = hbuf[(size_t)(row0+rl)*64+c];
-    os[idx] = o_out[(size_t)(row0+rl)*64+c];
-  }
-  __syncthreads();
-  if (t<192){
-    float a = bih[t];
-    #pragma unroll 8
-    for (int k=0;k<64;++k) a += smv_[k]*Wih[k*192+t];
-    sgi[t]=a;
-  }
-  __syncthreads();
-
-  const int c = t&63, rg = t>>6;
-  float o2a = bo[c], o2b = bo[c];
-  #pragma unroll 4
-  for (int k=0;k<64;++k){
-    float w = Wo[k*64+c];
-    o2a += os[(rg*2  )*64+k]*w;
-    o2b += os[(rg*2+1)*64+k]*w;
-  }
-  #pragma unroll
-  for (int i=0;i<2;++i){
-    int rl = rg*2 + i;
-    int row = row0 + rl;
-    float o2 = i ? o2b : o2a;
-    float hv = sa[rl*64+c];
-    float s2v = o2 + hv;
-    float ir = sgi[c]      + gh[(size_t)row*192+c];
-    float iz = sgi[64+c]   + gh[(size_t)row*192+64+c];
-    float inn = sgi[128+c];
-    float hn  = gh[(size_t)row*192+128+c];
-    float rr_ = sigmoidf_(ir);
-    float zz  = sigmoidf_(iz);
-    float nn  = tanhfast_(inn + rr_*hn);
-    float s1v = (1.f-zz)*nn + zz*hv + hv;
-    s1[(size_t)row*64+c] = s1v;
-    s2[(size_t)row*64+c] = s2v;
-    Sb1[rl*64+c] = s1v;
-    Sb2[rl*64+c] = s2v;
-  }
-  __syncthreads();
-  if (t<64){
-    float a=0.f,aq=0.f,b=0.f,bq2=0.f;
-    #pragma unroll
-    for (int rl=0;rl<8;++rl){
-      float v1 = Sb1[rl*64+t], v2 = Sb2[rl*64+t];
-      a+=v1; aq+=v1*v1; b+=v2; bq2+=v2*v2;
-    }
-    atomicAdd(&bnaccL[t],a);     atomicAdd(&bnaccL[64+t],aq);
-    atomicAdd(&bnaccL[128+t],b); atomicAdd(&bnaccL[192+t],bq2);
-  }
-}
-
-__global__ __launch_bounds__(256) void k_C(
-    const float* __restrict__ s1, const float* __restrict__ s2,
-    const float* __restrict__ bngL, const float* __restrict__ bnbL,
-    const float* __restrict__ W1, const float* __restrict__ b1,
-    const float* __restrict__ W2, const float* __restrict__ b2,
-    float* __restrict__ smlp, float* __restrict__ bnaccL)
-{
-  __shared__ float sa[8*64];
-  __shared__ float sh[8*128];
-  __shared__ float S2[8*64];
-  const int t = threadIdx.x, blk = blockIdx.x;
-  const int row0 = blk*8;
-
-  #pragma unroll
-  for (int i=0;i<2;++i){
-    int idx = t + 256*i;
-    int rl = idx>>6, c = idx&63;
-    int row = row0 + rl;
-    float mu1 = bnaccL[c]*(1.f/NB);
-    float va1 = bnaccL[64+c]*(1.f/NB) - mu1*mu1;
-    float mu2 = bnaccL[128+c]*(1.f/NB);
-    float va2 = bnaccL[192+c]*(1.f/NB) - mu2*mu2;
-    float h1 = bngL[c]*(s1[(size_t)row*64+c]-mu1)*rsqrtf(va1+1e-5f)+bnbL[c];
-    float h2 = bngL[64+c]*(s2[(size_t)row*64+c]-mu2)*rsqrtf(va2+1e-5f)+bnbL[64+c];
-    sa[idx] = h1+h2;
-  }
-  __syncthreads();
-  {
-    const int hj = t&127, rgq = t>>7;
-    float a0v=b1[hj], a1v=b1[hj], a2v=b1[hj], a3v=b1[hj];
-    #pragma unroll 4
-    for (int k=0;k<64;++k){
-      float w = W1[k*128+hj];
-      a0v += sa[(rgq*4  )*64+k]*w;
-      a1v += sa[(rgq*4+1)*64+k]*w;
-      a2v += sa[(rgq*4+2)*64+k]*w;
-      a3v += sa[(rgq*4+3)*64+k]*w;
-    }
-    sh[(rgq*4  )*128+hj] = fmaxf(a0v,0.f);
-    sh[(rgq*4+1)*128+hj] = fmaxf(a1v,0.f);
-    sh[(rgq*4+2)*128+hj] = fmaxf(a2v,0.f);
-    sh[(rgq*4+3)*128+hj] = fmaxf(a3v,0.f);
-  }
-  __syncthreads();
-  {
-    const int c = t&63, rg = t>>6;
-    float moa = b2[c], mob = b2[c];
-    #pragma unroll 4
-    for (int k=0;k<128;++k){
-      float w = W2[k*64+c];
-      moa += sh[(rg*2  )*128+k]*w;
-      mob += sh[(rg*2+1)*128+k]*w;
-    }
-    #pragma unroll
-    for (int i=0;i<2;++i){
-      int rl = rg*2+i;
-      float smv2 = sa[rl*64+c] + (i ? mob : moa);
-      smlp[(size_t)(row0+rl)*64+c] = smv2;
-      S2[rl*64+c] = smv2;
-    }
-  }
-  __syncthreads();
-  if (t<64){
-    float a=0.f,aq=0.f;
-    #pragma unroll
-    for (int rl=0;rl<8;++rl){ float v=S2[rl*64+t]; a+=v; aq+=v*v; }
-    atomicAdd(&bnaccL[256+t],a); atomicAdd(&bnaccL[320+t],aq);
-  }
-}
-
-__global__ __launch_bounds__(256) void k_out(
-  const float* __restrict__ smlp, const float* __restrict__ bnacc4,
-  const float* __restrict__ g4, const float* __restrict__ b4,
-  const float* __restrict__ outW, const float* __restrict__ outb,
-  float* __restrict__ out)
-{
-  __shared__ float hsT[64*20];
-  const int t = threadIdx.x, blk = blockIdx.x;
-  const int rg = blk>>2, cg = blk&3;
-  const int rows0 = rg*16;
-  #pragma unroll
-  for (int i=0;i<4;++i){
-    int idx = t + 256*i;
-    int k = idx&63, rr = idx>>6;
-    float mu = bnacc4[256+k]*(1.f/NB);
-    float va = bnacc4[320+k]*(1.f/NB)-mu*mu;
-    hsT[k*20+rr] = g4[k]*(smlp[(size_t)(rows0+rr)*64+k]-mu)*rsqrtf(va+1e-5f)+b4[k];
-  }
-  __syncthreads();
-  const int cc = cg*1024 + t*4;
-  float4 acc[16];
-  {
-    float4 bv = *(const float4*)&outb[cc];
-    #pragma unroll
-    for (int rr=0;rr<16;++rr) acc[rr]=bv;
-  }
-  #pragma unroll 4
-  for (int k=0;k<64;++k){
-    float4 w = *(const float4*)&outW[(size_t)k*4096+cc];
-    const float4* hp = (const float4*)&hsT[k*20];
-    float4 h0=hp[0], h1=hp[1], h2=hp[2], h3=hp[3];
-    acc[0].x+=h0.x*w.x;  acc[0].y+=h0.x*w.y;  acc[0].z+=h0.x*w.z;  acc[0].w+=h0.x*w.w;
-    acc[1].x+=h0.y*w.x;  acc[1].y+=h0.y*w.y;  acc[1].z+=h0.y*w.z;  acc[1].w+=h0.y*w.w;
-    acc[2].x+=h0.z*w.x;  acc[2].y+=h0.z*w.y;  acc[2].z+=h0.z*w.z;  acc[2].w+=h0.z*w.w;
-    acc[3].x+=h0.w*w.x;  acc[3].y+=h0.w*w.y;  acc[3].z+=h0.w*w.z;  acc[3].w+=h0.w*w.w;
-    acc[4].x+=h1.x*w.x;  acc[4].y+=h1.x*w.y;  acc[4].z+=h1.x*w.z;  acc[4].w+=h1.x*w.w;
-    acc[5].x+=h1.y*w.x;  acc[5].y+=h1.y*w.y;  acc[5].z+=h1.y*w.z;  acc[5].w+=h1.y*w.w;
-    acc[6].x+=h1.z*w.x;  acc[6].y+=h1.z*w.y;  acc[6].z+=h1.z*w.z;  acc[6].w+=h1.z*w.w;
-    acc[7].x+=h1.w*w.x;  acc[7].y+=h1.w*w.y;  acc[7].z+=h1.w*w.z;  acc[7].w+=h1.w*w.w;
-    acc[8].x+=h2.x*w.x;  acc[8].y+=h2.x*w.y;  acc[8].z+=h2.x*w.z;  acc[8].w+=h2.x*w.w;
-    acc[9].x+=h2.y*w.x;  acc[9].y+=h2.y*w.y;  acc[9].z+=h2.y*w.z;  acc[9].w+=h2.y*w.w;
-    acc[10].x+=h2.z*w.x; acc[10].y+=h2.z*w.y; acc[10].z+=h2.z*w.z; acc[10].w+=h2.z*w.w;
-    acc[11].x+=h2.w*w.x; acc[11].y+=h2.w*w.y; acc[11].z+=h2.w*w.z; acc[11].w+=h2.w*w.w;
-    acc[12].x+=h3.x*w.x; acc[12].y+=h3.x*w.y; acc[12].z+=h3.x*w.z; acc[12].w+=h3.x*w.w;
-    acc[13].x+=h3.y*w.x; acc[13].y+=h3.y*w.y; acc[13].z+=h3.y*w.z; acc[13].w+=h3.y*w.w;
-    acc[14].x+=h3.z*w.x; acc[14].y+=h3.z*w.y; acc[14].z+=h3.z*w.z; acc[14].w+=h3.z*w.w;
-    acc[15].x+=h3.w*w.x; acc[15].y+=h3.w*w.y; acc[15].z+=h3.w*w.z; acc[15].w+=h3.w*w.w;
-  }
-  #pragma unroll
-  for (int rr=0;rr<16;++rr)
-    *(float4*)&out[(size_t)(rows0+rr)*4096+cc] = acc[rr];
 }
 
 extern "C" void kernel_launch(void* const* d_in, const int* in_sizes, int n_in,
@@ -539,84 +463,40 @@
                               hipStream_t stream)
 {
   (void)in_sizes; (void)n_in; (void)out_size; (void)ws_size;
-  const float* x      = (const float*)d_in[0];
-  const float* tt     = (const float*)d_in[1];
-  const float* freqs  = (const float*)d_in[2];
-  const float* fc1W   = (const float*)d_in[3];
-  const float* fc1b   = (const float*)d_in[4];
-  const float* fc2W   = (const float*)d_in[5];
-  const float* fc2b   = (const float*)d_in[6];
-  const float* nodeW  = (const float*)d_in[7];
-  const float* nodeb  = (const float*)d_in[8];
-  const float* tprojW = (const float*)d_in[9];
-  const float* tprojb = (const float*)d_in[10];
-  const float* tcatW  = (const float*)d_in[11];
-  const float* tcatb  = (const float*)d_in[12];
-  const float* penb   = (const float*)d_in[14];
-  const float* pelW   = (const float*)d_in[15];
-  const float* pelb   = (const float*)d_in[16];
-  const float* catW   = (const float*)d_in[17];
-  const float* catb   = (const float*)d_in[18];
-  const float* convWg = (const float*)d_in[19];
-  const float* gruWih = (const float*)d_in[20];
-  const float* grubih = (const float*)d_in[21];
-  const float* gruWhh = (const float*)d_in[22];
-  const float* grubhh = (const float*)d_in[23];
-  const float* Wqkv   = (const float*)d_in[24];
-  const float* bqkv   = (const float*)d_in[25];
-  const float* Wo     = (const float*)d_in[26];
-  const float* bo     = (const float*)d_in[27];
-  const float* bng    = (const float*)d_in[28];
-  const float* bnb    = (const float*)d_in[29];
-  const float* W1     = (const float*)d_in[30];
-  const float* b1     = (const float*)d_in[31];
-  const float* W2     = (const float*)d_in[32];
-  const float* b2     = (const float*)d_in[33];
-  const float* outW   = (const float*)d_in[34];
-  const float* outb   = (const float*)d_in[35];
-
   float* ws = (float*)d_ws;
-  float* htime = ws;
-  float* hbuf  = htime + 131072;
-  float* gh    = hbuf + 131072;
-  float* s1    = gh + 393216;
-  float* s2    = s1 + 131072;
-  float* smlp  = s2 + 131072;
-  float* o_out = smlp + 131072;
-  float* hsum  = o_out + 131072;
-  float* bnacc = hsum + 320;
-  unsigned short* Qb = (unsigned short*)(bnacc + 1920);
-  unsigned short* Kb = Qb + 262144;
+  unsigned* cnt = (unsigned*)ws;
+  float* hsum  = ws + 64;
+  float* bnacc = ws + 128;
+  unsigned short* Kb = (unsigned short*)(ws + 2048);
   unsigned short* Vt = Kb + 262144;
-  float* h0p  = (float*)(Vt + 65536);
-
-  dim3 Blk(256);
-
-  k_pre<<<dim3(1024), Blk, 0, stream>>>(x, tt, freqs, fc1W, fc1b, fc2W, fc2b,
-                                        tprojW, tprojb, nodeW, h0p, htime, hsum);
-
-  k_assemble<<<dim3(512), Blk, 0, stream>>>(h0p, htime, nodeb, tcatW, tcatb,
-                                            penb, pelW, pelb, catW, catb, hbuf);
-
-  for (int l=0; l<NLAY; ++l){
-    const float* bnaccPrev = (l==0) ? bnacc : bnacc + (l-1)*384;
-    const float* gPrev = (l==0) ? bng : bng + (l-1)*192 + 128;
-    const float* bPrev = (l==0) ? bnb : bnb + (l-1)*192 + 128;
-    k_A<<<dim3(256), Blk, 0, stream>>>(smlp, bnaccPrev, gPrev, bPrev,
-                                       hbuf, hsum + l*64,
-                                       gruWhh + l*12288, grubhh + l*192,
-                                       Wqkv + l*12288, bqkv + l*192,
-                                       gh, Qb, Kb, Vt, (l==0) ? 1 : 0);
-    k_attn<<<dim3(512), Blk, 0, stream>>>(Qb, Kb, Vt, o_out);
-    k_B2<<<dim3(256), Blk, 0, stream>>>(hbuf, gh, hsum + l*64, o_out,
-                                        convWg + l*4096, gruWih + l*12288, grubih + l*192,
-                                        Wo + l*4096, bo + l*64,
-                                        s1, s2, bnacc + l*384);
-    k_C<<<dim3(256), Blk, 0, stream>>>(s1, s2, bng + l*192, bnb + l*192,
-                                       W1 + l*8192, b1 + l*128, W2 + l*8192, b2 + l*64,
-                                       smlp, bnacc + l*384);
-  }
-
-  k_out<<<dim3(512), Blk, 0, stream>>>(smlp, bnacc + 4*384, bng + 896, bnb + 896,
-                                       outW, outb, (float*)d_out);
+  float* h0p   = (float*)(Vt + 65536);
+  float* smlpG = h0p + 262144;
+
+  hipMemsetAsync(d_ws, 0, 2048*sizeof(float), stream);
+
+  MP p;
+  p.x = (const float*)d_in[0];   p.tt = (const float*)d_in[1];
+  p.freqs = (const float*)d_in[2];
+  p.fc1W = (const float*)d_in[3]; p.fc1b = (const float*)d_in[4];
+  p.fc2W = (const float*)d_in[5]; p.fc2b = (const float*)d_in[6];
+  p.nodeW = (const float*)d_in[7]; p.nodeb = (const float*)d_in[8];
+  p.tprojW = (const float*)d_in[9]; p.tprojb = (const float*)d_in[10];
+  p.tcatW = (const float*)d_in[11]; p.tcatb = (const float*)d_in[12];
+  p.penb = (const float*)d_in[14];
+  p.pelW = (const float*)d_in[15]; p.pelb = (const float*)d_in[16];
+  p.catW = (const float*)d_in[17]; p.catb = (const float*)d_in[18];
+  p.convWg = (const float*)d_in[19];
+  p.gruWih = (const float*)d_in[20]; p.grubih = (const float*)d_in[21];
+  p.gruWhh = (const float*)d_in[22]; p.grubhh = (const float*)d_in[23];
+  p.Wqkv = (const float*)d_in[24]; p.bqkv = (const float*)d_in[25];
+  p.Wo = (const float*)d_in[26];  p.bo = (const float*)d_in[27];
+  p.bng = (const float*)d_in[28]; p.bnb = (const float*)d_in[29];
+  p.W1 = (const float*)d_in[30];  p.b1 = (const float*)d_in[31];
+  p.W2 = (const float*)d_in[32];  p.b2 = (const float*)d_in[33];
+  p.outW = (const float*)d_in[34]; p.outb = (const float*)d_in[35];
+  p.out = (float*)d_out;
+  p.cnt = cnt; p.hsum = hsum; p.bnacc = bnacc;
+  p.Kb = Kb; p.Vt = Vt; p.h0p = h0p; p.smlpG = smlpG;
+
+  k_mega<<<dim3(256), dim3(512), 0, stream>>>(p);
 }
```

New measurement: 714.3 us. 36.4% more time.
